# Kernel tuning notes

Measured on AMD Instinct MI355X. Metric: run time of the kernel, lower is better.

The kernel has to match this reference:

```python
import jax, jax.numpy as jnp
import numpy as np

H = 256      # hidden_dim
NH = 4       # num_heads
DK = H // NH # per-head dim
NL = 2       # num self-attn layers
TL = 6       # transformer_num_layers (output repeat)
PTS_DIM = 3


def _layer_norm(x, g, b, eps=1e-5):
    m = jnp.mean(x, axis=-1, keepdims=True)
    v = jnp.mean((x - m) ** 2, axis=-1, keepdims=True)
    return (x - m) / jnp.sqrt(v + eps) * g + b


def _mha(x, Wq, bq, Wk, bk, Wv, bv, Wo, bo, g, bb, bias):
    # x: [B,N,H]; bias: [B,NH,N,N]; way='add' (att_spm_type='add')
    B, N, _ = x.shape
    q = (x @ Wq + bq).reshape(B, N, NH, DK).transpose(0, 2, 1, 3)  # [B,h,N,d]
    k = (x @ Wk + bk).reshape(B, N, NH, DK).transpose(0, 2, 1, 3)
    v = (x @ Wv + bv).reshape(B, N, NH, DK).transpose(0, 2, 1, 3)
    att = jnp.einsum('bhnd,bhmd->bhnm', q, k) / np.sqrt(DK).astype(np.float32)
    att = jax.nn.softmax(att + bias, axis=-1)
    out = jnp.einsum('bhnm,bhmd->bhnd', att, v).transpose(0, 2, 1, 3).reshape(B, N, H)
    out = out @ Wo + bo
    return _layer_norm(x + out, g, bb)


def setup_inputs() -> dict:
    key = jax.random.key(0)
    ks = jax.random.split(key, 16)
    B, N = 1, 512
    s = 0.02  # weight init scale
    inp = {
        'history_states': jax.random.normal(ks[0], (TL, B, N, H), jnp.float32),
        'all_lanes_preds': jax.random.normal(ks[1], (TL, B, N, 33), jnp.float32),
        'fc_W': jax.random.normal(ks[2], (H, H), jnp.float32) * s,
        'fc_b': jnp.zeros((H,), jnp.float32),
        'Wq': jax.random.normal(ks[3], (NL, H, H), jnp.float32) * s,
        'bq': jnp.zeros((NL, H), jnp.float32),
        'Wk': jax.random.normal(ks[4], (NL, H, H), jnp.float32) * s,
        'bk': jnp.zeros((NL, H), jnp.float32),
        'Wv': jax.random.normal(ks[5], (NL, H, H), jnp.float32) * s,
        'bv': jnp.zeros((NL, H), jnp.float32),
        'Wo': jax.random.normal(ks[6], (NL, H, H), jnp.float32) * s,
        'bo': jnp.zeros((NL, H), jnp.float32),
        'ln_g': jnp.ones((NL, H), jnp.float32),
        'ln_b': jnp.zeros((NL, H), jnp.float32),
        'mlp1_W': jax.random.normal(ks[7], (H, H), jnp.float32) * s,
        'mlp1_b': jnp.zeros((H,), jnp.float32),
        'mlp2_W': jax.random.normal(ks[8], (H, H), jnp.float32) * s,
        'mlp2_b': jnp.zeros((H,), jnp.float32),
        'cls_W1': jax.random.normal(ks[9], (2 * H, H), jnp.float32) * s,
        'cls_b1': jnp.zeros((H,), jnp.float32),
        'cls_W2': jax.random.normal(ks[10], (H, 1), jnp.float32) * s,
        'cls_b2': jnp.zeros((1,), jnp.float32),
    }
    return inp


def reference(history_states, all_lanes_preds, fc_W, fc_b, Wq, bq, Wk, bk, Wv, bv,
              Wo, bo, ln_g, ln_b, mlp1_W, mlp1_b, mlp2_W, mlp2_b,
              cls_W1, cls_b1, cls_W2, cls_b2):
    query_feats = history_states[-1]                 # [B,N,H]
    coords = all_lanes_preds[-1]                      # [B,N,33]
    B, N, C = coords.shape
    coords = coords.reshape(B, N, C // PTS_DIM, PTS_DIM)
    query_end_point = coords[:, :, -1, :]             # [B,N,3]
    key_start_point = coords[:, :, 0, :]              # [B,N,3]

    # pairwise distance bias: dist[b,i,j] = ||key_start[j] - query_end[i]||
    diff = key_start_point[:, None, :, :] - query_end_point[:, :, None, :]
    dist = jnp.sqrt(jnp.sum(diff ** 2, axis=-1))[:, None, :, :]  # [B,1,N,N]
    dw = 1.0 / (dist + 0.01)
    dw = dw / jnp.sum(dw, axis=2, keepdims=True)      # normalize over dim 2
    zeros = jnp.zeros_like(dw)
    dist_weights = jax.lax.stop_gradient(
        jnp.concatenate([dw, -dist, zeros, zeros], axis=1))  # [B,4,N,N]

    # features_concat: Linear + ReLU
    x = jax.nn.relu(query_feats @ fc_W + fc_b)

    for i in range(NL):
        x = _mha(x, Wq[i], bq[i], Wk[i], bk[i], Wv[i], bv[i],
                 Wo[i], bo[i], ln_g[i], ln_b[i], dist_weights)

    # lclc relationship head: per-side MLP, pairwise concat, classifier
    o1 = jax.nn.relu(x @ mlp1_W + mlp1_b)             # [B,N,H]
    o2 = jax.nn.relu(x @ mlp2_W + mlp2_b)
    pair = jnp.concatenate([
        jnp.broadcast_to(o1[:, :, None, :], (B, N, N, H)),
        jnp.broadcast_to(o2[:, None, :, :], (B, N, N, H))], axis=-1)  # [B,N,N,2H]
    z = jax.nn.relu(pair @ cls_W1 + cls_b1)
    lclc = (z @ cls_W2 + cls_b2)[..., 0]              # [B,N,N]
    all_lclc_preds = jnp.broadcast_to(lclc[None], (TL, B, N, N))
    return all_lclc_preds
```

## Files before the change

kernel.cpp:

```cpp
#include <hip/hip_runtime.h>
#include <math.h>


#define NTOK 512
#define HDIM 256
#define DKH  64
#define NHEAD 4
#define TLEN 6
#define SA 264
#define SQ 72

typedef __attribute__((ext_vector_type(8))) short bf16x8;
typedef __attribute__((ext_vector_type(4))) float f32x4;

struct GArg { const float* A; const float* W; const float* b; float* C; };

__device__ __forceinline__ ushort f2bf(float f)
{
    unsigned u = __builtin_bit_cast(unsigned, f);
    u += 0x7FFFu + ((u >> 16) & 1u);
    return (ushort)(u >> 16);
}

__device__ void prep_item(const float* __restrict__ pl, float* __restrict__ dist,
                          float* __restrict__ dwraw, float* __restrict__ inv_cs,
                          int item, float* smf)
{
    float* qe  = smf;
    float* red = smf + 1536;
    const int t = threadIdx.x;
    for (int i = t; i < 512; i += 256) {
        qe[i * 3 + 0] = pl[i * 33 + 30];
        qe[i * 3 + 1] = pl[i * 33 + 31];
        qe[i * 3 + 2] = pl[i * 33 + 32];
    }
    __syncthreads();
    const int m   = item * 64 + (t & 63);
    const int nch = t >> 6;
    const float kx = pl[m * 33 + 0], ky = pl[m * 33 + 1], kz = pl[m * 33 + 2];
    float cs = 0.f;
    for (int n = nch * 128; n < nch * 128 + 128; ++n) {
        const float dx = kx - qe[n * 3 + 0];
        const float dy = ky - qe[n * 3 + 1];
        const float dz = kz - qe[n * 3 + 2];
        const float dd = sqrtf(dx * dx + dy * dy + dz * dz);
        const float w  = 1.0f / (dd + 0.01f);
        dist[n * NTOK + m]  = dd;
        dwraw[n * NTOK + m] = w;
        cs += w;
    }
    red[nch * 64 + (t & 63)] = cs;
    __syncthreads();
    if (t < 64)
        inv_cs[item * 64 + t] =
            1.0f / (red[t] + red[64 + t] + red[128 + t] + red[192 + t]);
}

__global__ __launch_bounds__(256) void gemm_mfma(
    GArg g0, GArg g1, GArg g2, int relu, int aux, const float* __restrict__ pl,
    float* __restrict__ dist, float* __restrict__ dwraw,
    float* __restrict__ inv_cs)
{
    __shared__ __align__(16) ushort sm[2 * 64 * SA];
    const int bid = blockIdx.x;
    if (aux && bid >= 32) { prep_item(pl, dist, dwraw, inv_cs, bid - 32, (float*)sm); return; }

    const GArg ga  = (bid < 32) ? g0 : (bid < 64) ? g1 : g2;
    const int tile = bid & 31;
    const int row0 = (tile >> 2) * 64;
    const int col0 = (tile & 3) * 64;
    const int t    = threadIdx.x;
    ushort* As = sm;
    ushort* Ws = sm + 64 * SA;

#pragma unroll
    for (int j = 0; j < 16; ++j) {
        const int i = t + j * 256;
        const int r = i >> 6, c4 = i & 63;
        const float4 av = *(const float4*)&ga.A[(row0 + r) * HDIM + c4 * 4];
        ushort4 s;
        s.x = f2bf(av.x); s.y = f2bf(av.y); s.z = f2bf(av.z); s.w = f2bf(av.w);
        *(ushort4*)&As[r * SA + c4 * 4] = s;
    }
#pragma unroll
    for (int j = 0; j < 4; ++j) {
        const int i  = t + j * 256;
        const int cw = i & 15, kq = i >> 4;
        const float4 w0 = *(const float4*)&ga.W[(kq * 4 + 0) * HDIM + col0 + cw * 4];
        const float4 w1 = *(const float4*)&ga.W[(kq * 4 + 1) * HDIM + col0 + cw * 4];
        const float4 w2 = *(const float4*)&ga.W[(kq * 4 + 2) * HDIM + col0 + cw * 4];
        const float4 w3 = *(const float4*)&ga.W[(kq * 4 + 3) * HDIM + col0 + cw * 4];
        ushort4 s0 = {f2bf(w0.x), f2bf(w1.x), f2bf(w2.x), f2bf(w3.x)};
        ushort4 s1 = {f2bf(w0.y), f2bf(w1.y), f2bf(w2.y), f2bf(w3.y)};
        ushort4 s2 = {f2bf(w0.z), f2bf(w1.z), f2bf(w2.z), f2bf(w3.z)};
        ushort4 s3 = {f2bf(w0.w), f2bf(w1.w), f2bf(w2.w), f2bf(w3.w)};
        *(ushort4*)&Ws[(cw * 4 + 0) * SA + kq * 4] = s0;
        *(ushort4*)&Ws[(cw * 4 + 1) * SA + kq * 4] = s1;
        *(ushort4*)&Ws[(cw * 4 + 2) * SA + kq * 4] = s2;
        *(ushort4*)&Ws[(cw * 4 + 3) * SA + kq * 4] = s3;
    }
    __syncthreads();

    const int wv = t >> 6, lane = t & 63;
    const int frow = lane & 15;
    const int fk   = (lane >> 4) * 8;
    const ushort* Arow = As + (wv * 16 + frow) * SA + fk;
    const ushort* Wrow = Ws + frow * SA + fk;

    f32x4 acc[4];
#pragma unroll
    for (int j = 0; j < 4; ++j) acc[j] = (f32x4){0.f, 0.f, 0.f, 0.f};

#pragma unroll
    for (int ks = 0; ks < 8; ++ks) {
        const bf16x8 a = *(const bf16x8*)&Arow[ks * 32];
#pragma unroll
        for (int j = 0; j < 4; ++j) {
            const bf16x8 b = *(const bf16x8*)&Wrow[j * 16 * SA + ks * 32];
            acc[j] = __builtin_amdgcn_mfma_f32_16x16x32_bf16(a, b, acc[j], 0, 0, 0);
        }
    }

    const int orow = row0 + wv * 16 + (lane >> 4) * 4;
    const int ocol = col0 + (lane & 15);
#pragma unroll
    for (int j = 0; j < 4; ++j) {
        const int col = ocol + j * 16;
        const float bb = ga.b ? ga.b[col] : 0.f;
#pragma unroll
        for (int rg = 0; rg < 4; ++rg) {
            float o = acc[j][rg] + bb;
            if (relu) o = fmaxf(o, 0.f);
            ga.C[(orow + rg) * HDIM + col] = o;
        }
    }
}

__global__ __launch_bounds__(256) void qkt_mfma(
    const float* __restrict__ q, const float* __restrict__ k,
    const float* __restrict__ dist, const float* __restrict__ dwraw,
    const float* __restrict__ inv_cs, float* __restrict__ S)
{
    __shared__ __align__(16) ushort Qs[64 * SQ];
    __shared__ __align__(16) ushort Ks[64 * SQ];

    const int h  = blockIdx.z;
    const int n0 = blockIdx.y * 64;
    const int m0 = blockIdx.x * 64;
    const int t  = threadIdx.x;

#pragma unroll
    for (int j = 0; j < 4; ++j) {
        const int i = t + j * 256;
        const int r = i >> 4, c4 = i & 15;
        const float4 qv = *(const float4*)&q[(n0 + r) * HDIM + h * DKH + c4 * 4];
        ushort4 sq = {f2bf(qv.x), f2bf(qv.y), f2bf(qv.z), f2bf(qv.w)};
        *(ushort4*)&Qs[r * SQ + c4 * 4] = sq;
        const float4 kv = *(const float4*)&k[(m0 + r) * HDIM + h * DKH + c4 * 4];
        ushort4 sk = {f2bf(kv.x), f2bf(kv.y), f2bf(kv.z), f2bf(kv.w)};
        *(ushort4*)&Ks[r * SQ + c4 * 4] = sk;
    }
    __syncthreads();

    const int wv = t >> 6, lane = t & 63;
    const int frow = lane & 15;
    const int fk   = (lane >> 4) * 8;
    const ushort* Qrow = Qs + (wv * 16 + frow) * SQ + fk;
    const ushort* Krow = Ks + frow * SQ + fk;

    f32x4 acc[4];
#pragma unroll
    for (int j = 0; j < 4; ++j) acc[j] = (f32x4){0.f, 0.f, 0.f, 0.f};

#pragma unroll
    for (int ks = 0; ks < 2; ++ks) {
        const bf16x8 a = *(const bf16x8*)&Qrow[ks * 32];
#pragma unroll
        for (int j = 0; j < 4; ++j) {
            const bf16x8 b = *(const bf16x8*)&Krow[j * 16 * SQ + ks * 32];
            acc[j] = __builtin_amdgcn_mfma_f32_16x16x32_bf16(a, b, acc[j], 0, 0, 0);
        }
    }

    const int orow = n0 + wv * 16 + (lane >> 4) * 4;
    const int ocol = m0 + (lane & 15);
#pragma unroll
    for (int j = 0; j < 4; ++j) {
        const int m  = ocol + j * 16;
        const float ic = (h == 0) ? inv_cs[m] : 0.f;
#pragma unroll
        for (int rg = 0; rg < 4; ++rg) {
            const int n = orow + rg;
            float bias = 0.f;
            if (h == 0)      bias = dwraw[n * NTOK + m] * ic;
            else if (h == 1) bias = -dist[n * NTOK + m];
            S[(h * NTOK + n) * NTOK + m] = acc[j][rg] * 0.125f + bias;
        }
    }
}

__global__ __launch_bounds__(256) void smpv_kernel(
    const float* __restrict__ S, const float* __restrict__ v,
    float* __restrict__ ao)
{
    __shared__ float ps[NTOK * 10];
    __shared__ float ri[8];
    __shared__ __align__(16) float exch[4 * 8 * 16 * 4];

    const int h  = blockIdx.y;
    const int n0 = blockIdx.x * 8;
    const int t  = threadIdx.x;

    {
        const int row = t >> 5, j = t & 31;
        const float* Srow = S + (h * NTOK + n0 + row) * NTOK;
        float vals[16];
        float mx = -1e30f;
#pragma unroll
        for (int u = 0; u < 16; ++u) {
            vals[u] = Srow[j + u * 32];
            mx = fmaxf(mx, vals[u]);
        }
#pragma unroll
        for (int o = 16; o; o >>= 1) mx = fmaxf(mx, __shfl_xor(mx, o, 32));
        float sum = 0.f;
#pragma unroll
        for (int u = 0; u < 16; ++u) {
            const float e = __expf(vals[u] - mx);
            vals[u] = e;
            sum += e;
        }
#pragma unroll
        for (int o = 16; o; o >>= 1) sum += __shfl_xor(sum, o, 32);
        if (j == 0) ri[row] = 1.0f / sum;
#pragma unroll
        for (int u = 0; u < 16; ++u)
            ps[(j + u * 32) * 10 + row] = vals[u];
    }
    __syncthreads();

    const int tx = t & 15, rp = (t >> 4) & 3, kh = t >> 6;
    const int r0 = rp * 2;
    const float* vb = v + (kh * 128) * HDIM + h * DKH + tx * 4;
    f32x4 a0 = {0.f, 0.f, 0.f, 0.f}, a1 = {0.f, 0.f, 0.f, 0.f};
#pragma unroll 8
    for (int kk = 0; kk < 128; ++kk) {
        const float4 vv = *(const float4*)&vb[kk * HDIM];
        const float2 pp = *(const float2*)&ps[(kh * 128 + kk) * 10 + r0];
        a0.x += pp.x * vv.x; a0.y += pp.x * vv.y;
        a0.z += pp.x * vv.z; a0.w += pp.x * vv.w;
        a1.x += pp.y * vv.x; a1.y += pp.y * vv.y;
        a1.z += pp.y * vv.z; a1.w += pp.y * vv.w;
    }
    if (kh > 0) {
        *(f32x4*)&exch[((kh * 8 + r0) * 16 + tx) * 4]     = a0;
        *(f32x4*)&exch[((kh * 8 + r0 + 1) * 16 + tx) * 4] = a1;
    }
    __syncthreads();
    if (kh == 0) {
#pragma unroll
        for (int kk = 1; kk < 4; ++kk) {
            const f32x4 e0 = *(const f32x4*)&exch[((kk * 8 + r0) * 16 + tx) * 4];
            const f32x4 e1 = *(const f32x4*)&exch[((kk * 8 + r0 + 1) * 16 + tx) * 4];
            a0 += e0; a1 += e1;
        }
        const float s0 = ri[r0], s1 = ri[r0 + 1];
        float4 o0, o1;
        o0.x = a0.x * s0; o0.y = a0.y * s0; o0.z = a0.z * s0; o0.w = a0.w * s0;
        o1.x = a1.x * s1; o1.y = a1.y * s1; o1.z = a1.z * s1; o1.w = a1.w * s1;
        *(float4*)&ao[(n0 + r0) * HDIM + h * DKH + tx * 4]     = o0;
        *(float4*)&ao[(n0 + r0 + 1) * HDIM + h * DKH + tx * 4] = o1;
    }
}

__global__ __launch_bounds__(256) void resid_ln(const float* __restrict__ proj,
                                                const float* __restrict__ g,
                                                const float* __restrict__ b,
                                                float* __restrict__ x)
{
    const int n = blockIdx.x, t = threadIdx.x;
    __shared__ float red[4];
    const float y = x[n * HDIM + t] + proj[n * HDIM + t];
    float s = y;
#pragma unroll
    for (int o = 32; o; o >>= 1) s += __shfl_xor(s, o);
    if ((t & 63) == 0) red[t >> 6] = s;
    __syncthreads();
    const float mean = (red[0] + red[1] + red[2] + red[3]) * (1.0f / HDIM);
    const float c = y - mean;
    float s2 = c * c;
#pragma unroll
    for (int o = 32; o; o >>= 1) s2 += __shfl_xor(s2, o);
    __syncthreads();
    if ((t & 63) == 0) red[t >> 6] = s2;
    __syncthreads();
    const float var = (red[0] + red[1] + red[2] + red[3]) * (1.0f / HDIM);
    x[n * HDIM + t] = c * rsqrtf(var + 1e-5f) * g[t] + b[t];
}

__global__ __launch_bounds__(256) void pair_cls(const float* __restrict__ U1,
                                                const float* __restrict__ U2,
                                                const float* __restrict__ W2,
                                                const float* __restrict__ b2,
                                                float* __restrict__ out)
{
    __shared__ __align__(16) float u1s[32][260];
    __shared__ __align__(16) float u2s[32][260];
    __shared__ __align__(16) float w2s[256];
    const int t  = threadIdx.x;
    const int n0 = blockIdx.y * 32, m0 = blockIdx.x * 32;

    for (int i = t; i < 32 * 64; i += 256) {
        const int r = i >> 6, c4 = i & 63;
        *(float4*)&u1s[r][c4 * 4] = *(const float4*)&U1[(n0 + r) * HDIM + c4 * 4];
        *(float4*)&u2s[r][c4 * 4] = *(const float4*)&U2[(m0 + r) * HDIM + c4 * 4];
    }
    if (t < 64) *(float4*)&w2s[t * 4] = *(const float4*)&W2[t * 4];
    __syncthreads();

    const int tx = t & 15, ty = t >> 4;
    float acc[2][2] = {};
    for (int h4 = 0; h4 < 64; ++h4) {
        const float4 a0 = *(const float4*)&u1s[ty * 2][h4 * 4];
        const float4 a1 = *(const float4*)&u1s[ty * 2 + 1][h4 * 4];
        const float4 b0 = *(const float4*)&u2s[tx * 2][h4 * 4];
        const float4 b1 = *(const float4*)&u2s[tx * 2 + 1][h4 * 4];
        const float4 w  = *(const float4*)&w2s[h4 * 4];
#define RT(A, B) fmaxf((A) + (B), 0.f)
        acc[0][0] += RT(a0.x,b0.x)*w.x + RT(a0.y,b0.y)*w.y + RT(a0.z,b0.z)*w.z + RT(a0.w,b0.w)*w.w;
        acc[0][1] += RT(a0.x,b1.x)*w.x + RT(a0.y,b1.y)*w.y + RT(a0.z,b1.z)*w.z + RT(a0.w,b1.w)*w.w;
        acc[1][0] += RT(a1.x,b0.x)*w.x + RT(a1.y,b0.y)*w.y + RT(a1.z,b0.z)*w.z + RT(a1.w,b0.w)*w.w;
        acc[1][1] += RT(a1.x,b1.x)*w.x + RT(a1.y,b1.y)*w.y + RT(a1.z,b1.z)*w.z + RT(a1.w,b1.w)*w.w;
#undef RT
    }
    const float bb = b2[0];
#pragma unroll
    for (int ii = 0; ii < 2; ++ii)
#pragma unroll
        for (int jj = 0; jj < 2; ++jj) {
            const float val = acc[ii][jj] + bb;
            const int n = n0 + ty * 2 + ii;
            const int m = m0 + tx * 2 + jj;
#pragma unroll
            for (int tl = 0; tl < TLEN; ++tl)
                out[tl * NTOK * NTOK + n * NTOK + m] = val;
        }
}

extern "C" void kernel_launch(void* const* d_in, const int* in_sizes, int n_in,
                              void* d_out, int out_size, void* d_ws, size_t ws_size,
                              hipStream_t stream)
{
    const float* hs   = (const float*)d_in[0];
    const float* qf   = hs + 5 * NTOK * HDIM;
    const float* alp  = (const float*)d_in[1];
    const float* pl   = alp + 5 * NTOK * 33;
    const float* fc_W = (const float*)d_in[2];
    const float* fc_b = (const float*)d_in[3];
    const float* Wq   = (const float*)d_in[4];
    const float* bq   = (const float*)d_in[5];
    const float* Wk   = (const float*)d_in[6];
    const float* bk   = (const float*)d_in[7];
    const float* Wv   = (const float*)d_in[8];
    const float* bv   = (const float*)d_in[9];
    const float* Wo   = (const float*)d_in[10];
    const float* bo   = (const float*)d_in[11];
    const float* lng  = (const float*)d_in[12];
    const float* lnb  = (const float*)d_in[13];
    const float* m1W  = (const float*)d_in[14];
    const float* m1b  = (const float*)d_in[15];
    const float* m2W  = (const float*)d_in[16];
    const float* m2b  = (const float*)d_in[17];
    const float* cW1  = (const float*)d_in[18];
    const float* cb1  = (const float*)d_in[19];
    const float* cW2  = (const float*)d_in[20];
    const float* cb2  = (const float*)d_in[21];
    float* out = (float*)d_out;

    const int NN  = NTOK * NTOK;
    const int NH_ = NTOK * HDIM;
    float* ws     = (float*)d_ws;
    float* dist   = ws;
    float* dwraw  = ws + NN;
    float* inv_cs = ws + 2 * NN;
    float* x      = ws + 2 * NN + 512;
    float* v      = x + NH_;
    float* ao     = v + NH_;
    float* q      = ao + NH_;
    float* k      = q + NH_;
    float* S      = k + NH_;

    const GArg gz = {nullptr, nullptr, nullptr, nullptr};

    gemm_mfma<<<40, 256, 0, stream>>>(
        GArg{qf, fc_W, fc_b, x}, gz, gz, 1, 1, pl, dist, dwraw, inv_cs);

    for (int L = 0; L < 2; ++L) {
        const float* wq = Wq + L * HDIM * HDIM;
        const float* wk = Wk + L * HDIM * HDIM;
        const float* wv = Wv + L * HDIM * HDIM;
        const float* wo = Wo + L * HDIM * HDIM;

        gemm_mfma<<<96, 256, 0, stream>>>(
            GArg{x, wq, bq + L * HDIM, q}, GArg{x, wk, bk + L * HDIM, k},
            GArg{x, wv, bv + L * HDIM, v}, 0, 0, pl, dist, dwraw, inv_cs);

        qkt_mfma<<<dim3(8, 8, NHEAD), 256, 0, stream>>>(
            q, k, dist, dwraw, inv_cs, S);
        smpv_kernel<<<dim3(64, NHEAD), 256, 0, stream>>>(S, v, ao);
        gemm_mfma<<<32, 256, 0, stream>>>(
            GArg{ao, wo, bo + L * HDIM, q}, gz, gz, 0, 0, pl, dist, dwraw, inv_cs);
        resid_ln<<<NTOK, 256, 0, stream>>>(q, lng + L * HDIM, lnb + L * HDIM, x);
    }

    gemm_mfma<<<64, 256, 0, stream>>>(
        GArg{x, m1W, m1b, q}, GArg{x, m2W, m2b, k}, gz, 1, 0,
        pl, dist, dwraw, inv_cs);
    gemm_mfma<<<64, 256, 0, stream>>>(
        GArg{q, cW1, cb1, v}, GArg{k, cW1 + HDIM * HDIM, nullptr, ao}, gz, 0, 0,
        pl, dist, dwraw, inv_cs);

    pair_cls<<<dim3(16, 16), 256, 0, stream>>>(v, ao, cW2, cb2, out);
}
```

Measured before the change: 113.8 us.

## Prepack bf16 weights once, keep activations in bf16, fuse O-proj with LayerNorm

A new pack kernel converts all 13 weight matrices to transposed bf16 and converts the query features to bf16, alongside the distance precompute. The GEMMs then read bf16 operands straight from global memory with no shared-memory staging or per-tile conversion, and producers write bf16 copies of q, k, x and the attention output. The output projection is fused with the residual add and LayerNorm in one single-wave-per-16-rows kernel, which removes the resid_ln launch. This cuts redundant fp32 loads and conversions and one kernel, but adds a pack launch each call and gives up LDS reuse for operands.

```diff
diff --git a/kernel.cpp b/kernel.cpp
--- a/kernel.cpp
+++ b/kernel.cpp
@@ -7,13 +7,10 @@
 #define DKH  64
 #define NHEAD 4
 #define TLEN 6
-#define SA 264
-#define SQ 72
+#define WSZ  65536
 
 typedef __attribute__((ext_vector_type(8))) short bf16x8;
 typedef __attribute__((ext_vector_type(4))) float f32x4;
-
-struct GArg { const float* A; const float* W; const float* b; float* C; };
 
 __device__ __forceinline__ ushort f2bf(float f)
 {
@@ -22,90 +19,101 @@
     return (ushort)(u >> 16);
 }
 
-__device__ void prep_item(const float* __restrict__ pl, float* __restrict__ dist,
-                          float* __restrict__ dwraw, float* __restrict__ inv_cs,
-                          int item, float* smf)
-{
-    float* qe  = smf;
-    float* red = smf + 1536;
+struct PKArg {
+    const float* w[13];
+    const float* qf; const float* pl;
+    ushort* wpk; ushort* qf16;
+    float *dist, *dwraw, *inv_cs;
+};
+
+__global__ __launch_bounds__(256) void pack_kernel(PKArg p)
+{
+    __shared__ __align__(16) ushort smu[64 * 72];
+    const int bid = blockIdx.x;
+    const int t   = threadIdx.x;
+
+    if (bid < 208) {
+        const int mat  = bid >> 4;
+        const int tile = bid & 15;
+        const int k0   = (tile >> 2) * 64;
+        const int c0   = (tile & 3) * 64;
+        const float* W = p.w[mat];
+#pragma unroll
+        for (int j = 0; j < 4; ++j) {
+            const int i  = t + j * 256;
+            const int r  = i >> 4, c4 = i & 15;
+            const float4 v4 = *(const float4*)&W[(k0 + r) * HDIM + c0 + c4 * 4];
+            smu[(c4 * 4 + 0) * 72 + r] = f2bf(v4.x);
+            smu[(c4 * 4 + 1) * 72 + r] = f2bf(v4.y);
+            smu[(c4 * 4 + 2) * 72 + r] = f2bf(v4.z);
+            smu[(c4 * 4 + 3) * 72 + r] = f2bf(v4.w);
+        }
+        __syncthreads();
+#pragma unroll
+        for (int j = 0; j < 2; ++j) {
+            const int i  = t + j * 256;
+            const int cr = i >> 3, kk = i & 7;
+            const uint4 v = *(const uint4*)&smu[cr * 72 + kk * 8];
+            *(uint4*)&p.wpk[mat * WSZ + (c0 + cr) * HDIM + k0 + kk * 8] = v;
+        }
+    } else if (bid < 224) {
+        const int r0 = (bid - 208) * 32;
+#pragma unroll
+        for (int j = 0; j < 8; ++j) {
+            const int i  = t + j * 256;
+            const int r  = i >> 6, c4 = i & 63;
+            const float4 v4 = *(const float4*)&p.qf[(r0 + r) * HDIM + c4 * 4];
+            ushort4 s = {f2bf(v4.x), f2bf(v4.y), f2bf(v4.z), f2bf(v4.w)};
+            *(ushort4*)&p.qf16[(r0 + r) * HDIM + c4 * 4] = s;
+        }
+    } else {
+        float* smf = (float*)smu;
+        float* qe  = smf;
+        float* red = smf + 1536;
+        const int item = bid - 224;
+        for (int i = t; i < 512; i += 256) {
+            qe[i * 3 + 0] = p.pl[i * 33 + 30];
+            qe[i * 3 + 1] = p.pl[i * 33 + 31];
+            qe[i * 3 + 2] = p.pl[i * 33 + 32];
+        }
+        __syncthreads();
+        const int m   = item * 64 + (t & 63);
+        const int nch = t >> 6;
+        const float kx = p.pl[m * 33 + 0], ky = p.pl[m * 33 + 1], kz = p.pl[m * 33 + 2];
+        float cs = 0.f;
+        for (int n = nch * 128; n < nch * 128 + 128; ++n) {
+            const float dx = kx - qe[n * 3 + 0];
+            const float dy = ky - qe[n * 3 + 1];
+            const float dz = kz - qe[n * 3 + 2];
+            const float dd = sqrtf(dx * dx + dy * dy + dz * dz);
+            const float w  = 1.0f / (dd + 0.01f);
+            p.dist[n * NTOK + m]  = dd;
+            p.dwraw[n * NTOK + m] = w;
+            cs += w;
+        }
+        red[nch * 64 + (t & 63)] = cs;
+        __syncthreads();
+        if (t < 64)
+            p.inv_cs[item * 64 + t] =
+                1.0f / (red[t] + red[64 + t] + red[128 + t] + red[192 + t]);
+    }
+}
+
+struct GB { const ushort* A16; const ushort* Wt; const float* b;
+            float* C; ushort* C16; };
+
+__global__ __launch_bounds__(256) void gemm_bf(GB g0, GB g1, GB g2, int relu)
+{
+    const int bid = blockIdx.x;
+    const GB g = (bid < 32) ? g0 : (bid < 64) ? g1 : g2;
     const int t = threadIdx.x;
-    for (int i = t; i < 512; i += 256) {
-        qe[i * 3 + 0] = pl[i * 33 + 30];
-        qe[i * 3 + 1] = pl[i * 33 + 31];
-        qe[i * 3 + 2] = pl[i * 33 + 32];
-    }
-    __syncthreads();
-    const int m   = item * 64 + (t & 63);
-    const int nch = t >> 6;
-    const float kx = pl[m * 33 + 0], ky = pl[m * 33 + 1], kz = pl[m * 33 + 2];
-    float cs = 0.f;
-    for (int n = nch * 128; n < nch * 128 + 128; ++n) {
-        const float dx = kx - qe[n * 3 + 0];
-        const float dy = ky - qe[n * 3 + 1];
-        const float dz = kz - qe[n * 3 + 2];
-        const float dd = sqrtf(dx * dx + dy * dy + dz * dz);
-        const float w  = 1.0f / (dd + 0.01f);
-        dist[n * NTOK + m]  = dd;
-        dwraw[n * NTOK + m] = w;
-        cs += w;
-    }
-    red[nch * 64 + (t & 63)] = cs;
-    __syncthreads();
-    if (t < 64)
-        inv_cs[item * 64 + t] =
-            1.0f / (red[t] + red[64 + t] + red[128 + t] + red[192 + t]);
-}
-
-__global__ __launch_bounds__(256) void gemm_mfma(
-    GArg g0, GArg g1, GArg g2, int relu, int aux, const float* __restrict__ pl,
-    float* __restrict__ dist, float* __restrict__ dwraw,
-    float* __restrict__ inv_cs)
-{
-    __shared__ __align__(16) ushort sm[2 * 64 * SA];
-    const int bid = blockIdx.x;
-    if (aux && bid >= 32) { prep_item(pl, dist, dwraw, inv_cs, bid - 32, (float*)sm); return; }
-
-    const GArg ga  = (bid < 32) ? g0 : (bid < 64) ? g1 : g2;
-    const int tile = bid & 31;
-    const int row0 = (tile >> 2) * 64;
-    const int col0 = (tile & 3) * 64;
-    const int t    = threadIdx.x;
-    ushort* As = sm;
-    ushort* Ws = sm + 64 * SA;
-
-#pragma unroll
-    for (int j = 0; j < 16; ++j) {
-        const int i = t + j * 256;
-        const int r = i >> 6, c4 = i & 63;
-        const float4 av = *(const float4*)&ga.A[(row0 + r) * HDIM + c4 * 4];
-        ushort4 s;
-        s.x = f2bf(av.x); s.y = f2bf(av.y); s.z = f2bf(av.z); s.w = f2bf(av.w);
-        *(ushort4*)&As[r * SA + c4 * 4] = s;
-    }
-#pragma unroll
-    for (int j = 0; j < 4; ++j) {
-        const int i  = t + j * 256;
-        const int cw = i & 15, kq = i >> 4;
-        const float4 w0 = *(const float4*)&ga.W[(kq * 4 + 0) * HDIM + col0 + cw * 4];
-        const float4 w1 = *(const float4*)&ga.W[(kq * 4 + 1) * HDIM + col0 + cw * 4];
-        const float4 w2 = *(const float4*)&ga.W[(kq * 4 + 2) * HDIM + col0 + cw * 4];
-        const float4 w3 = *(const float4*)&ga.W[(kq * 4 + 3) * HDIM + col0 + cw * 4];
-        ushort4 s0 = {f2bf(w0.x), f2bf(w1.x), f2bf(w2.x), f2bf(w3.x)};
-        ushort4 s1 = {f2bf(w0.y), f2bf(w1.y), f2bf(w2.y), f2bf(w3.y)};
-        ushort4 s2 = {f2bf(w0.z), f2bf(w1.z), f2bf(w2.z), f2bf(w3.z)};
-        ushort4 s3 = {f2bf(w0.w), f2bf(w1.w), f2bf(w2.w), f2bf(w3.w)};
-        *(ushort4*)&Ws[(cw * 4 + 0) * SA + kq * 4] = s0;
-        *(ushort4*)&Ws[(cw * 4 + 1) * SA + kq * 4] = s1;
-        *(ushort4*)&Ws[(cw * 4 + 2) * SA + kq * 4] = s2;
-        *(ushort4*)&Ws[(cw * 4 + 3) * SA + kq * 4] = s3;
-    }
-    __syncthreads();
-
     const int wv = t >> 6, lane = t & 63;
-    const int frow = lane & 15;
-    const int fk   = (lane >> 4) * 8;
-    const ushort* Arow = As + (wv * 16 + frow) * SA + fk;
-    const ushort* Wrow = Ws + frow * SA + fk;
+    const int gw = (bid & 31) * 4 + wv;
+    const int rg = gw >> 2, cg = gw & 3;
+    const int lr = lane & 15, lk = (lane >> 4) * 8;
+
+    const ushort* Arow = g.A16 + (rg * 16 + lr) * HDIM + lk;
+    const ushort* Wrow = g.Wt + (cg * 64 + lr) * HDIM + lk;
 
     f32x4 acc[4];
 #pragma unroll
@@ -116,57 +124,42 @@
         const bf16x8 a = *(const bf16x8*)&Arow[ks * 32];
 #pragma unroll
         for (int j = 0; j < 4; ++j) {
-            const bf16x8 b = *(const bf16x8*)&Wrow[j * 16 * SA + ks * 32];
+            const bf16x8 b = *(const bf16x8*)&Wrow[j * 16 * HDIM + ks * 32];
             acc[j] = __builtin_amdgcn_mfma_f32_16x16x32_bf16(a, b, acc[j], 0, 0, 0);
         }
     }
 
-    const int orow = row0 + wv * 16 + (lane >> 4) * 4;
-    const int ocol = col0 + (lane & 15);
+    const int orow = rg * 16 + (lane >> 4) * 4;
 #pragma unroll
     for (int j = 0; j < 4; ++j) {
-        const int col = ocol + j * 16;
-        const float bb = ga.b ? ga.b[col] : 0.f;
-#pragma unroll
-        for (int rg = 0; rg < 4; ++rg) {
-            float o = acc[j][rg] + bb;
+        const int col = cg * 64 + j * 16 + lr;
+        const float bb = g.b ? g.b[col] : 0.f;
+#pragma unroll
+        for (int r = 0; r < 4; ++r) {
+            float o = acc[j][r] + bb;
             if (relu) o = fmaxf(o, 0.f);
-            ga.C[(orow + rg) * HDIM + col] = o;
-        }
-    }
-}
-
-__global__ __launch_bounds__(256) void qkt_mfma(
-    const float* __restrict__ q, const float* __restrict__ k,
+            if (g.C)   g.C[(orow + r) * HDIM + col] = o;
+            if (g.C16) g.C16[(orow + r) * HDIM + col] = f2bf(o);
+        }
+    }
+}
+
+__global__ __launch_bounds__(256) void qkt_bf(
+    const ushort* __restrict__ q16, const ushort* __restrict__ k16,
     const float* __restrict__ dist, const float* __restrict__ dwraw,
     const float* __restrict__ inv_cs, float* __restrict__ S)
 {
-    __shared__ __align__(16) ushort Qs[64 * SQ];
-    __shared__ __align__(16) ushort Ks[64 * SQ];
-
-    const int h  = blockIdx.z;
-    const int n0 = blockIdx.y * 64;
-    const int m0 = blockIdx.x * 64;
+    const int bid = blockIdx.x;
+    const int h  = bid >> 6;
+    const int ng = (bid >> 1) & 31;
+    const int mh = bid & 1;
     const int t  = threadIdx.x;
-
-#pragma unroll
-    for (int j = 0; j < 4; ++j) {
-        const int i = t + j * 256;
-        const int r = i >> 4, c4 = i & 15;
-        const float4 qv = *(const float4*)&q[(n0 + r) * HDIM + h * DKH + c4 * 4];
-        ushort4 sq = {f2bf(qv.x), f2bf(qv.y), f2bf(qv.z), f2bf(qv.w)};
-        *(ushort4*)&Qs[r * SQ + c4 * 4] = sq;
-        const float4 kv = *(const float4*)&k[(m0 + r) * HDIM + h * DKH + c4 * 4];
-        ushort4 sk = {f2bf(kv.x), f2bf(kv.y), f2bf(kv.z), f2bf(kv.w)};
-        *(ushort4*)&Ks[r * SQ + c4 * 4] = sk;
-    }
-    __syncthreads();
-
     const int wv = t >> 6, lane = t & 63;
-    const int frow = lane & 15;
-    const int fk   = (lane >> 4) * 8;
-    const ushort* Qrow = Qs + (wv * 16 + frow) * SQ + fk;
-    const ushort* Krow = Ks + frow * SQ + fk;
+    const int m0 = mh * 256 + wv * 64;
+    const int lr = lane & 15, lk = (lane >> 4) * 8;
+
+    const ushort* Qrow = q16 + (ng * 16 + lr) * HDIM + h * DKH + lk;
+    const ushort* Krow = k16 + (m0 + lr) * HDIM + h * DKH + lk;
 
     f32x4 acc[4];
 #pragma unroll
@@ -177,31 +170,30 @@
         const bf16x8 a = *(const bf16x8*)&Qrow[ks * 32];
 #pragma unroll
         for (int j = 0; j < 4; ++j) {
-            const bf16x8 b = *(const bf16x8*)&Krow[j * 16 * SQ + ks * 32];
+            const bf16x8 b = *(const bf16x8*)&Krow[j * 16 * HDIM + ks * 32];
             acc[j] = __builtin_amdgcn_mfma_f32_16x16x32_bf16(a, b, acc[j], 0, 0, 0);
         }
     }
 
-    const int orow = n0 + wv * 16 + (lane >> 4) * 4;
-    const int ocol = m0 + (lane & 15);
+    const int orow = ng * 16 + (lane >> 4) * 4;
 #pragma unroll
     for (int j = 0; j < 4; ++j) {
-        const int m  = ocol + j * 16;
+        const int m = m0 + j * 16 + lr;
         const float ic = (h == 0) ? inv_cs[m] : 0.f;
 #pragma unroll
-        for (int rg = 0; rg < 4; ++rg) {
-            const int n = orow + rg;
+        for (int r = 0; r < 4; ++r) {
+            const int n = orow + r;
             float bias = 0.f;
             if (h == 0)      bias = dwraw[n * NTOK + m] * ic;
             else if (h == 1) bias = -dist[n * NTOK + m];
-            S[(h * NTOK + n) * NTOK + m] = acc[j][rg] * 0.125f + bias;
+            S[(h * NTOK + n) * NTOK + m] = acc[j][r] * 0.125f + bias;
         }
     }
 }
 
 __global__ __launch_bounds__(256) void smpv_kernel(
     const float* __restrict__ S, const float* __restrict__ v,
-    float* __restrict__ ao)
+    ushort* __restrict__ ao16)
 {
     __shared__ float ps[NTOK * 10];
     __shared__ float ri[8];
@@ -260,42 +252,83 @@
     if (kh == 0) {
 #pragma unroll
         for (int kk = 1; kk < 4; ++kk) {
-            const f32x4 e0 = *(const f32x4*)&exch[((kk * 8 + r0) * 16 + tx) * 4];
-            const f32x4 e1 = *(const f32x4*)&exch[((kk * 8 + r0 + 1) * 16 + tx) * 4];
-            a0 += e0; a1 += e1;
+            a0 += *(const f32x4*)&exch[((kk * 8 + r0) * 16 + tx) * 4];
+            a1 += *(const f32x4*)&exch[((kk * 8 + r0 + 1) * 16 + tx) * 4];
         }
         const float s0 = ri[r0], s1 = ri[r0 + 1];
-        float4 o0, o1;
-        o0.x = a0.x * s0; o0.y = a0.y * s0; o0.z = a0.z * s0; o0.w = a0.w * s0;
-        o1.x = a1.x * s1; o1.y = a1.y * s1; o1.z = a1.z * s1; o1.w = a1.w * s1;
-        *(float4*)&ao[(n0 + r0) * HDIM + h * DKH + tx * 4]     = o0;
-        *(float4*)&ao[(n0 + r0 + 1) * HDIM + h * DKH + tx * 4] = o1;
-    }
-}
-
-__global__ __launch_bounds__(256) void resid_ln(const float* __restrict__ proj,
-                                                const float* __restrict__ g,
-                                                const float* __restrict__ b,
-                                                float* __restrict__ x)
-{
-    const int n = blockIdx.x, t = threadIdx.x;
-    __shared__ float red[4];
-    const float y = x[n * HDIM + t] + proj[n * HDIM + t];
-    float s = y;
-#pragma unroll
-    for (int o = 32; o; o >>= 1) s += __shfl_xor(s, o);
-    if ((t & 63) == 0) red[t >> 6] = s;
-    __syncthreads();
-    const float mean = (red[0] + red[1] + red[2] + red[3]) * (1.0f / HDIM);
-    const float c = y - mean;
-    float s2 = c * c;
-#pragma unroll
-    for (int o = 32; o; o >>= 1) s2 += __shfl_xor(s2, o);
-    __syncthreads();
-    if ((t & 63) == 0) red[t >> 6] = s2;
-    __syncthreads();
-    const float var = (red[0] + red[1] + red[2] + red[3]) * (1.0f / HDIM);
-    x[n * HDIM + t] = c * rsqrtf(var + 1e-5f) * g[t] + b[t];
+        ushort4 o0 = {f2bf(a0.x * s0), f2bf(a0.y * s0), f2bf(a0.z * s0), f2bf(a0.w * s0)};
+        ushort4 o1 = {f2bf(a1.x * s1), f2bf(a1.y * s1), f2bf(a1.z * s1), f2bf(a1.w * s1)};
+        *(ushort4*)&ao16[(n0 + r0) * HDIM + h * DKH + tx * 4]     = o0;
+        *(ushort4*)&ao16[(n0 + r0 + 1) * HDIM + h * DKH + tx * 4] = o1;
+    }
+}
+
+__global__ __launch_bounds__(64) void oprojln(
+    const ushort* __restrict__ ao16, const ushort* __restrict__ WoT,
+    const float* __restrict__ bo, const float* __restrict__ g,
+    const float* __restrict__ bb, float* __restrict__ x,
+    ushort* __restrict__ x16)
+{
+    const int rg = blockIdx.x;
+    const int lane = threadIdx.x;
+    const int lr = lane & 15, lk = (lane >> 4) * 8;
+
+    const ushort* Arow = ao16 + (rg * 16 + lr) * HDIM + lk;
+    const ushort* Brow = WoT + lr * HDIM + lk;
+
+    f32x4 acc[16];
+#pragma unroll
+    for (int j = 0; j < 16; ++j) acc[j] = (f32x4){0.f, 0.f, 0.f, 0.f};
+
+#pragma unroll
+    for (int ks = 0; ks < 8; ++ks) {
+        const bf16x8 a = *(const bf16x8*)&Arow[ks * 32];
+#pragma unroll
+        for (int j = 0; j < 16; ++j) {
+            const bf16x8 b = *(const bf16x8*)&Brow[j * 16 * HDIM + ks * 32];
+            acc[j] = __builtin_amdgcn_mfma_f32_16x16x32_bf16(a, b, acc[j], 0, 0, 0);
+        }
+    }
+
+    const int row0 = rg * 16 + (lane >> 4) * 4;
+#pragma unroll
+    for (int j = 0; j < 16; ++j) {
+        const int col = j * 16 + lr;
+        const float bc = bo[col];
+#pragma unroll
+        for (int r = 0; r < 4; ++r)
+            acc[j][r] += bc + x[(row0 + r) * HDIM + col];
+    }
+    float mean[4], rstd[4];
+#pragma unroll
+    for (int r = 0; r < 4; ++r) {
+        float s = 0.f;
+#pragma unroll
+        for (int j = 0; j < 16; ++j) s += acc[j][r];
+#pragma unroll
+        for (int o = 8; o; o >>= 1) s += __shfl_xor(s, o);
+        mean[r] = s * (1.0f / 256.0f);
+        float s2 = 0.f;
+#pragma unroll
+        for (int j = 0; j < 16; ++j) {
+            const float c = acc[j][r] - mean[r];
+            s2 += c * c;
+        }
+#pragma unroll
+        for (int o = 8; o; o >>= 1) s2 += __shfl_xor(s2, o);
+        rstd[r] = rsqrtf(s2 * (1.0f / 256.0f) + 1e-5f);
+    }
+#pragma unroll
+    for (int j = 0; j < 16; ++j) {
+        const int col = j * 16 + lr;
+        const float gg = g[col], bv = bb[col];
+#pragma unroll
+        for (int r = 0; r < 4; ++r) {
+            const float o = (acc[j][r] - mean[r]) * rstd[r] * gg + bv;
+            x[(row0 + r) * HDIM + col]   = o;
+            x16[(row0 + r) * HDIM + col] = f2bf(o);
+        }
+    }
 }
 
 __global__ __launch_bounds__(256) void pair_cls(const float* __restrict__ U1,
@@ -333,12 +366,12 @@
         acc[1][1] += RT(a1.x,b1.x)*w.x + RT(a1.y,b1.y)*w.y + RT(a1.z,b1.z)*w.z + RT(a1.w,b1.w)*w.w;
 #undef RT
     }
-    const float bb = b2[0];
+    const float bbv = b2[0];
 #pragma unroll
     for (int ii = 0; ii < 2; ++ii)
 #pragma unroll
         for (int jj = 0; jj < 2; ++jj) {
-            const float val = acc[ii][jj] + bb;
+            const float val = acc[ii][jj] + bbv;
             const int n = n0 + ty * 2 + ii;
             const int m = m0 + tx * 2 + jj;
 #pragma unroll
@@ -385,40 +418,60 @@
     float* inv_cs = ws + 2 * NN;
     float* x      = ws + 2 * NN + 512;
     float* v      = x + NH_;
-    float* ao     = v + NH_;
-    float* q      = ao + NH_;
-    float* k      = q + NH_;
-    float* S      = k + NH_;
-
-    const GArg gz = {nullptr, nullptr, nullptr, nullptr};
-
-    gemm_mfma<<<40, 256, 0, stream>>>(
-        GArg{qf, fc_W, fc_b, x}, gz, gz, 1, 1, pl, dist, dwraw, inv_cs);
+    float* U1     = v + NH_;
+    float* U2     = U1 + NH_;
+    float* S      = U2 + NH_;
+    ushort* u16   = (ushort*)(S + 4 * NN);
+    ushort* wpk   = u16;
+    ushort* qf16  = wpk + 13 * WSZ;
+    ushort* x16   = qf16 + NH_;
+    ushort* q16   = x16 + NH_;
+    ushort* k16   = q16 + NH_;
+    ushort* ao16  = k16 + NH_;
+    ushort* o116  = ao16 + NH_;
+    ushort* o216  = o116 + NH_;
+
+    PKArg pk;
+    pk.w[0]  = fc_W;
+    pk.w[1]  = Wq;  pk.w[2]  = Wq + WSZ;
+    pk.w[3]  = Wk;  pk.w[4]  = Wk + WSZ;
+    pk.w[5]  = Wv;  pk.w[6]  = Wv + WSZ;
+    pk.w[7]  = Wo;  pk.w[8]  = Wo + WSZ;
+    pk.w[9]  = m1W; pk.w[10] = m2W;
+    pk.w[11] = cW1; pk.w[12] = cW1 + WSZ;
+    pk.qf = qf; pk.pl = pl;
+    pk.wpk = wpk; pk.qf16 = qf16;
+    pk.dist = dist; pk.dwraw = dwraw; pk.inv_cs = inv_cs;
+    pack_kernel<<<232, 256, 0, stream>>>(pk);
+
+    const GB gzb = {nullptr, nullptr, nullptr, nullptr, nullptr};
+
+    gemm_bf<<<32, 256, 0, stream>>>(
+        GB{qf16, wpk + 0 * WSZ, fc_b, x, x16}, gzb, gzb, 1);
 
     for (int L = 0; L < 2; ++L) {
-        const float* wq = Wq + L * HDIM * HDIM;
-        const float* wk = Wk + L * HDIM * HDIM;
-        const float* wv = Wv + L * HDIM * HDIM;
-        const float* wo = Wo + L * HDIM * HDIM;
-
-        gemm_mfma<<<96, 256, 0, stream>>>(
-            GArg{x, wq, bq + L * HDIM, q}, GArg{x, wk, bk + L * HDIM, k},
-            GArg{x, wv, bv + L * HDIM, v}, 0, 0, pl, dist, dwraw, inv_cs);
-
-        qkt_mfma<<<dim3(8, 8, NHEAD), 256, 0, stream>>>(
-            q, k, dist, dwraw, inv_cs, S);
-        smpv_kernel<<<dim3(64, NHEAD), 256, 0, stream>>>(S, v, ao);
-        gemm_mfma<<<32, 256, 0, stream>>>(
-            GArg{ao, wo, bo + L * HDIM, q}, gz, gz, 0, 0, pl, dist, dwraw, inv_cs);
-        resid_ln<<<NTOK, 256, 0, stream>>>(q, lng + L * HDIM, lnb + L * HDIM, x);
-    }
-
-    gemm_mfma<<<64, 256, 0, stream>>>(
-        GArg{x, m1W, m1b, q}, GArg{x, m2W, m2b, k}, gz, 1, 0,
-        pl, dist, dwraw, inv_cs);
-    gemm_mfma<<<64, 256, 0, stream>>>(
-        GArg{q, cW1, cb1, v}, GArg{k, cW1 + HDIM * HDIM, nullptr, ao}, gz, 0, 0,
-        pl, dist, dwraw, inv_cs);
-
-    pair_cls<<<dim3(16, 16), 256, 0, stream>>>(v, ao, cW2, cb2, out);
-}
+        const ushort* wq = wpk + (1 + L) * WSZ;
+        const ushort* wk = wpk + (3 + L) * WSZ;
+        const ushort* wv = wpk + (5 + L) * WSZ;
+        const ushort* wo = wpk + (7 + L) * WSZ;
+
+        gemm_bf<<<96, 256, 0, stream>>>(
+            GB{x16, wq, bq + L * HDIM, nullptr, q16},
+            GB{x16, wk, bk + L * HDIM, nullptr, k16},
+            GB{x16, wv, bv + L * HDIM, v, nullptr}, 0);
+
+        qkt_bf<<<256, 256, 0, stream>>>(q16, k16, dist, dwraw, inv_cs, S);
+        smpv_kernel<<<dim3(64, NHEAD), 256, 0, stream>>>(S, v, ao16);
+        oprojln<<<32, 64, 0, stream>>>(
+            ao16, wo, bo + L * HDIM, lng + L * HDIM, lnb + L * HDIM, x, x16);
+    }
+
+    gemm_bf<<<64, 256, 0, stream>>>(
+        GB{x16, wpk + 9 * WSZ, m1b, nullptr, o116},
+        GB{x16, wpk + 10 * WSZ, m2b, nullptr, o216}, gzb, 1);
+    gemm_bf<<<64, 256, 0, stream>>>(
+        GB{o116, wpk + 11 * WSZ, cb1, U1, nullptr},
+        GB{o216, wpk + 12 * WSZ, nullptr, U2, nullptr}, gzb, 0);
+
+    pair_cls<<<dim3(16, 16), 256, 0, stream>>>(U1, U2, cW2, cb2, out);
+}
```

After: 128.0 us. 1.12x slower.
